# Optimization experiments

Measured on AMD Instinct MI355X. Metric: run time of the kernel, lower is better.

## Reference

```python
import jax, jax.numpy as jnp
import numpy as np

N = 100000
E = 1600000
D = 128  # out_dim == head_dim (num_heads = 1)


def setup_inputs() -> dict:
    key = jax.random.key(0)
    ks = jax.random.split(key, 16)
    s = 0.05
    inp = {
        "h": jax.random.normal(ks[0], (N, D), dtype=jnp.float32),
        "c": jax.random.normal(ks[1], (N, 3), dtype=jnp.float32),
        "src": jax.random.randint(ks[2], (E,), 0, N),
        "dst": jax.random.randint(ks[3], (E,), 0, N),
        # Q/K/V projections (use_bias=False)
        "Wq": jax.random.normal(ks[4], (D, D), dtype=jnp.float32) * s,
        "Wk": jax.random.normal(ks[5], (D, D), dtype=jnp.float32) * s,
        "Wv": jax.random.normal(ks[6], (D, D), dtype=jnp.float32) * s,
        # linear_p: Linear(3,3) -> ReLU -> Linear(3,D)
        "Wp1": jax.random.normal(ks[7], (3, 3), dtype=jnp.float32) * s,
        "bp1": jnp.zeros((3,), dtype=jnp.float32),
        "Wp2": jax.random.normal(ks[8], (3, D), dtype=jnp.float32) * s,
        "bp2": jnp.zeros((D,), dtype=jnp.float32),
        # edge MLP: Linear(D,D) -> ReLU -> Linear(D,1)
        "We1": jax.random.normal(ks[9], (D, D), dtype=jnp.float32) * s,
        "be1": jnp.zeros((D,), dtype=jnp.float32),
        "We2": jax.random.normal(ks[10], (D, 1), dtype=jnp.float32) * s,
        "be2": jnp.zeros((1,), dtype=jnp.float32),
        # output projection O (has bias)
        "Wo": jax.random.normal(ks[11], (D, D), dtype=jnp.float32) * s,
        "bo": jnp.zeros((D,), dtype=jnp.float32),
    }
    return inp


def reference(h, c, src, dst, Wq, Wk, Wv, Wp1, bp1, Wp2, bp2,
              We1, be1, We2, be2, Wo, bo):
    scale = np.sqrt(np.float32(D))  # sqrt(out_dim) used by scaled_exp
    n = h.shape[0]
    # node projections
    Q = h @ Wq                                   # [N, D]
    K = h @ Wk                                   # [N, D]
    V = h @ Wv                                   # [N, D]
    P = jax.nn.relu(c @ Wp1 + bp1) @ Wp2 + bp2   # [N, D] position encoding
    # per-edge point-transformer score: MLP(K[src] - Q[dst] + P[src])
    dif = K[src] - Q[dst] + P[src]               # [E, D]
    raw = jax.nn.relu(dif @ We1 + be1) @ We2 + be2  # [E, 1]
    score = jnp.exp(jnp.clip(raw / scale, -5.0, 5.0))  # [E, 1]
    # gather-multiply-scatter: weighted V+P sum and normalizer z per dst node
    msg = (V + P)[src] * score                   # [E, D]
    wV = jax.ops.segment_sum(msg, dst, num_segments=n)    # [N, D]
    z = jax.ops.segment_sum(score, dst, num_segments=n)   # [N, 1]
    head_out = wV / z                            # [N, D]
    return head_out @ Wo + bo                    # [N, D]
```

## Files before the change

### kernel.cpp

```cpp
#include <hip/hip_runtime.h>
#include <math.h>

#define DD 128
#define CAP 10240
#define KVS 272
typedef unsigned int u32;
typedef unsigned short u16;
typedef __attribute__((ext_vector_type(8))) short bf16x8;
typedef __attribute__((ext_vector_type(4))) float f32x4;
typedef __attribute__((ext_vector_type(2))) float f32x2;

__device__ __forceinline__ float4 f4zero() { return make_float4(0.f, 0.f, 0.f, 0.f); }
__device__ __forceinline__ u32 bf16rne(float f) {
    u32 u = __float_as_uint(f);
    u += 0x7FFFu + ((u >> 16) & 1u);
    return u >> 16;
}
__device__ __forceinline__ u32 pack2(float lo, float hi) {
    return bf16rne(lo) | (bf16rne(hi) << 16);
}
__device__ __forceinline__ float unlo(u32 u) { return __uint_as_float(u << 16); }
__device__ __forceinline__ float unhi(u32 u) { return __uint_as_float(u & 0xFFFF0000u); }
__device__ __forceinline__ float ub0(u32 v) { return (float)(v & 0xFFu); }
__device__ __forceinline__ float ub1(u32 v) { return (float)((v >> 8) & 0xFFu); }
__device__ __forceinline__ float ub2(u32 v) { return (float)((v >> 16) & 0xFFu); }
__device__ __forceinline__ float ub3(u32 v) { return (float)(v >> 24); }

__global__ __launch_bounds__(256) void fused_pre(
    const float* __restrict__ Wq, const float* __restrict__ Wk,
    const float* __restrict__ Wv, const float* __restrict__ We1,
    const float* __restrict__ be1, const float* __restrict__ Wp2,
    const float* __restrict__ bp2, const float* __restrict__ Wo,
    u32* __restrict__ BF,
    const int* __restrict__ src, const int* __restrict__ dst,
    int* __restrict__ gcount, u32* __restrict__ ebuf, int E) {
    const int t = threadIdx.x;
    if (blockIdx.x < 30) {
        const int bid = blockIdx.x * 4 + (t >> 6);
        const int l = t & 63;
        const int c = l & 15;
        const int kg = l >> 4;
        float val[8];

        const int ct = bid / 5, ks = bid - ct * 5;
        const int u = ct / 6, r = ct - u * 6;
        const int n = 32 * u + 16 * (r < 2 ? r : (r & 1)) + c;
#pragma unroll
        for (int j = 0; j < 8; ++j) {
            const int k = ks * 32 + kg * 8 + j;
            float v = 0.f;
            if (r < 2) {
                if (k < 128) {
                    float a = 0.f;
                    for (int q = 0; q < 128; ++q)
                        a = fmaf(Wq[k * 128 + q], We1[q * 128 + n], a);
                    v = a;
                }
            } else if (r < 4) {
                if (k < 128) {
                    float a = 0.f;
                    for (int q = 0; q < 128; ++q)
                        a = fmaf(Wk[k * 128 + q], We1[q * 128 + n], a);
                    v = a;
                } else if (k < 131) {
                    float a = 0.f;
                    for (int q = 0; q < 128; ++q)
                        a = fmaf(Wp2[(k - 128) * 128 + q], We1[q * 128 + n], a);
                    v = a;
                } else if (k == 131) {
                    float a = be1[n];
                    for (int q = 0; q < 128; ++q)
                        a = fmaf(bp2[q], We1[q * 128 + n], a);
                    v = a;
                }
            } else {
                if (k < 128) {
                    float a = 0.f;
                    for (int q = 0; q < 128; ++q)
                        a = fmaf(Wv[k * 128 + q], Wo[q * 128 + n], a);
                    v = a;
                } else if (k < 131) {
                    float a = 0.f;
                    for (int q = 0; q < 128; ++q)
                        a = fmaf(Wp2[(k - 128) * 128 + q], Wo[q * 128 + n], a);
                    v = a;
                } else if (k == 131) {
                    float a = 0.f;
                    for (int q = 0; q < 128; ++q)
                        a = fmaf(bp2[q], Wo[q * 128 + n], a);
                    v = a;
                }
            }
            val[j] = v;
        }
        u32* dp = &BF[((size_t)bid * 64 + l) * 4];
        dp[0] = pack2(val[0], val[1]);
        dp[1] = pack2(val[2], val[3]);
        dp[2] = pack2(val[4], val[5]);
        dp[3] = pack2(val[6], val[7]);
    } else {
        __shared__ int hist[256];
        __shared__ int base[256];
        hist[t] = 0;
        __syncthreads();
        const int chunk = (blockIdx.x - 30) * 4096;
        int bk[16], rk[16];
        u32 pv[16];
#pragma unroll
        for (int i = 0; i < 16; ++i) {
            int idx = chunk + i * 256 + t;
            bk[i] = -1;
            if (idx < E) {
                int dd = dst[idx];
                int ss = src[idx];
                bk[i] = dd >> 9;
                pv[i] = ((u32)ss << 9) | (u32)(dd & 511);
                rk[i] = atomicAdd(&hist[bk[i]], 1);
            }
        }
        __syncthreads();
        if (hist[t]) base[t] = t * CAP + atomicAdd(&gcount[t], hist[t]);
        __syncthreads();
#pragma unroll
        for (int i = 0; i < 16; ++i) {
            if (bk[i] >= 0) ebuf[base[bk[i]] + rk[i]] = pv[i];
        }
    }
}

__global__ __launch_bounds__(256) void scanB_we2r(
    const int* __restrict__ gcount, int* __restrict__ bucket_base,
    const float* __restrict__ We2, float* __restrict__ We2r) {
    __shared__ int s[256];
    int t = threadIdx.x;
    int orig = gcount[t];
    s[t] = orig;
    __syncthreads();
    for (int off = 1; off < 256; off <<= 1) {
        int x = (t >= off) ? s[t - off] : 0;
        __syncthreads();
        s[t] += x;
        __syncthreads();
    }
    bucket_base[t] = s[t] - orig;
    if (t < 128) {
        int col = 32 * (t >> 5) + 16 * (t & 1) + ((t & 31) >> 1);
        We2r[t] = We2[col];
    }
}

__global__ __launch_bounds__(256) void fused_mid(
    const float* __restrict__ h, const float* __restrict__ c,
    const float* __restrict__ Wp1, const float* __restrict__ bp1,
    const u32* __restrict__ BF,
    u32* __restrict__ QWb, unsigned char* __restrict__ KV, int N,
    const int* __restrict__ gcount, const int* __restrict__ bucket_base,
    const u32* __restrict__ ebuf, int* __restrict__ ssrc,
    int* __restrict__ offs, int E, int NR) {
    __shared__ u32 lds[64 * 96];
    const int t = threadIdx.x;

    if ((int)blockIdx.x < NR) {
        int* cnt = (int*)lds;
        int* cur = cnt + 512;
        int* ts = cur + 512;
        const int r = blockIdx.x;
        const int cnt_r = gcount[r];
        const int base_r = bucket_base[r];
        cnt[t] = 0;
        cnt[t + 256] = 0;
        __syncthreads();
        const u32* eb = &ebuf[(size_t)r * CAP];
        for (int i = t; i < cnt_r; i += 256) atomicAdd(&cnt[eb[i] & 511], 1);
        __syncthreads();
        int v0 = cnt[2 * t], v1 = cnt[2 * t + 1];
        int pair = v0 + v1;
        ts[t] = pair;
        __syncthreads();
        for (int off = 1; off < 256; off <<= 1) {
            int x = (t >= off) ? ts[t - off] : 0;
            __syncthreads();
            ts[t] += x;
            __syncthreads();
        }
        int ex = ts[t] - pair;
        cur[2 * t] = ex;
        cur[2 * t + 1] = ex + v0;
        offs[r * 512 + 2 * t] = base_r + ex;
        offs[r * 512 + 2 * t + 1] = base_r + ex + v0;
        if (r == NR - 1 && t == 255) offs[NR * 512] = E;
        __syncthreads();
        for (int i = t; i < cnt_r; i += 256) {
            u32 e = eb[i];
            int p = atomicAdd(&cur[e & 511], 1);
            ssrc[base_r + p] = (int)(e >> 9);
        }
    } else {
        u32* hs = lds;
        const int row0 = ((int)blockIdx.x - NR) * 64;

#pragma unroll
        for (int i = 0; i < 8; ++i) {
            int f = t + i * 256;
            int row = f >> 5;
            int cq = f & 31;
            float4 v = f4zero();
            if (row0 + row < N) v = *(const float4*)&h[(size_t)(row0 + row) * DD + cq * 4];
            int idx = row * 96 + ((cq * 2) ^ ((row & 7) << 2));
            uint2 p;
            p.x = pack2(v.x, v.y);
            p.y = pack2(v.z, v.w);
            *(uint2*)&hs[idx] = p;
        }
        if (t < 64) {
            int row = t;
            float u0 = 0.f, u1 = 0.f, u2 = 0.f;
            if (row0 + row < N) {
                const float* cr = &c[(size_t)(row0 + row) * 3];
                float c0 = cr[0], c1 = cr[1], c2 = cr[2];
                u0 = fmaxf(bp1[0] + c0 * Wp1[0] + c1 * Wp1[3] + c2 * Wp1[6], 0.f);
                u1 = fmaxf(bp1[1] + c0 * Wp1[1] + c1 * Wp1[4] + c2 * Wp1[7], 0.f);
                u2 = fmaxf(bp1[2] + c0 * Wp1[2] + c1 * Wp1[5] + c2 * Wp1[8], 0.f);
            }
            int swz = (row & 7) << 2;
            uint4 z0 = make_uint4(pack2(u0, u1), pack2(u2, 1.0f), 0u, 0u);
            uint4 zz = make_uint4(0u, 0u, 0u, 0u);
#pragma unroll
            for (int q = 0; q < 4; ++q) {
                int idx = row * 96 + 64 + ((q * 4) ^ swz);
                *(uint4*)&hs[idx] = (q == 0) ? z0 : zz;
            }
        }
        __syncthreads();

        const int w = t >> 6, l = t & 63;
        const int cc = l & 15, kg = l >> 4;

        f32x4 acc[4][6];
#pragma unroll
        for (int rt = 0; rt < 4; ++rt)
#pragma unroll
            for (int r = 0; r < 6; ++r) acc[rt][r] = (f32x4){0.f, 0.f, 0.f, 0.f};

#pragma unroll
        for (int ks = 0; ks < 5; ++ks) {
            bf16x8 a[4];
#pragma unroll
            for (int rt = 0; rt < 4; ++rt) {
                int row = rt * 16 + cc;
                int idx = row * 96 + ((ks * 16 + kg * 4) ^ ((row & 7) << 2));
                a[rt] = *(const bf16x8*)&hs[idx];
            }
#pragma unroll
            for (int r = 0; r < 6; ++r) {
                const bf16x8 b = *(const bf16x8*)&BF[(((size_t)(w * 6 + r) * 5 + ks) * 64 + l) * 4];
#pragma unroll
                for (int rt = 0; rt < 4; ++rt)
                    acc[rt][r] = __builtin_amdgcn_mfma_f32_16x16x32_bf16(a[rt], b, acc[rt][r], 0, 0, 0);
            }
        }

        __syncthreads();
        if (t < 64) hs[t] = 0u;
        __syncthreads();
#pragma unroll
        for (int rt = 0; rt < 4; ++rt) {
#pragma unroll
            for (int j = 0; j < 4; ++j) {
                int rl = rt * 16 + kg * 4 + j;
                float m = fmaxf(fabsf(acc[rt][4][j]), fabsf(acc[rt][5][j]));
                atomicMax((int*)&hs[rl], __float_as_int(m));
            }
        }
        __syncthreads();

#pragma unroll
        for (int rt = 0; rt < 4; ++rt) {
#pragma unroll
            for (int j = 0; j < 4; ++j) {
                int rl = rt * 16 + kg * 4 + j;
                int row = row0 + rl;
                if (row >= N) continue;
                float smax = __int_as_float((int)hs[rl]);
                float scale = (smax > 0.f) ? smax * (1.0f / 127.0f) : 1.0f;
                float rsc = 1.0f / scale;
                QWb[(size_t)row * 64 + w * 16 + cc] = pack2(acc[rt][0][j], acc[rt][1][j]);
                unsigned char* kvrow = &KV[(size_t)row * KVS];
                u32 kp = __builtin_amdgcn_cvt_pk_fp8_f32(acc[rt][2][j], acc[rt][3][j], 0u, false);
                *(u16*)&kvrow[w * 32 + cc * 2] = (u16)kp;
                int q0 = (int)rintf(acc[rt][4][j] * rsc) + 128;
                int q1 = (int)rintf(acc[rt][5][j] * rsc) + 128;
                *(u16*)&kvrow[128 + 2 * (w * 16 + cc)] = (u16)((q0 & 0xFF) | ((q1 & 0xFF) << 8));
                if (w == 0 && cc == 0) *(float*)&kvrow[256] = scale;
            }
        }
    }
}

__global__ __launch_bounds__(256) void aggregate(
    const int* __restrict__ offs, const int* __restrict__ ssrc,
    const unsigned char* __restrict__ KV, const u32* __restrict__ QWb,
    const float* __restrict__ We2r, const float* __restrict__ be2,
    const float* __restrict__ bo, float* __restrict__ out, int N) {
    const int node = (blockIdx.x * 256 + threadIdx.x) >> 6;
    const int lane = threadIdx.x & 63;
    if (node >= N) return;
    const int g = lane >> 4, i = lane & 15;

    const float SC = 0.08838834764831845f * 1.4426950408889634f;
    const float CL = 5.0f * 1.4426950408889634f;

    uint4 Qu = *(const uint4*)&QWb[(size_t)node * 64 + 4 * i];
    f32x2 q01 = {unlo(Qu.x), unhi(Qu.x)};
    f32x2 q23 = {unlo(Qu.y), unhi(Qu.y)};
    f32x2 q45 = {unlo(Qu.z), unhi(Qu.z)};
    f32x2 q67 = {unlo(Qu.w), unhi(Qu.w)};
    f32x2 w01 = *(const f32x2*)&We2r[8 * i];
    f32x2 w23 = *(const f32x2*)&We2r[8 * i + 2];
    f32x2 w45 = *(const f32x2*)&We2r[8 * i + 4];
    f32x2 w67 = *(const f32x2*)&We2r[8 * i + 6];
    const float B2SC = be2[0] * SC;
    const f32x2 zero2 = {0.f, 0.f};

    const int beg = offs[node], end = offs[node + 1];
    float a0 = 0.f, a1 = 0.f, a2 = 0.f, a3 = 0.f;
    float a4 = 0.f, a5 = 0.f, a6 = 0.f, a7 = 0.f;
    float zacc = 0.f, zs = 0.f;

    int e = beg + g;
    int s = (e < end) ? ssrc[e] : 0;
    for (int e0 = beg; e0 < end; e0 += 4) {
        const bool act = (e0 + g) < end;
        const unsigned char* row = &KV[(size_t)s * KVS];
        uint2 kk = *(const uint2*)&row[8 * i];
        uint2 vv = *(const uint2*)&row[128 + 8 * i];
        float scl = *(const float*)&row[256];
        int en = e0 + 4 + g;
        s = (en < end) ? ssrc[en] : 0;

        f32x2 d, p2;
        d = __builtin_amdgcn_cvt_pk_f32_fp8(kk.x, false) - q01;
        d = __builtin_elementwise_max(d, zero2);
        p2 = d * w01;
        d = __builtin_amdgcn_cvt_pk_f32_fp8(kk.x, true) - q23;
        d = __builtin_elementwise_max(d, zero2);
        p2 += d * w23;
        d = __builtin_amdgcn_cvt_pk_f32_fp8(kk.y, false) - q45;
        d = __builtin_elementwise_max(d, zero2);
        p2 += d * w45;
        d = __builtin_amdgcn_cvt_pk_f32_fp8(kk.y, true) - q67;
        d = __builtin_elementwise_max(d, zero2);
        p2 += d * w67;
        float p = p2[0] + p2[1];
#pragma unroll
        for (int off = 1; off <= 8; off <<= 1) p += __shfl_xor(p, off);

        float targ = fmaf(p, SC, B2SC);
        targ = fminf(fmaxf(targ, -CL), CL);
        float sc = act ? exp2f(targ) : 0.f;
        float scsc = sc * scl;
        zacc += sc;
        zs += scsc;

        a0 = fmaf(ub0(vv.x), scsc, a0);
        a1 = fmaf(ub1(vv.x), scsc, a1);
        a2 = fmaf(ub2(vv.x), scsc, a2);
        a3 = fmaf(ub3(vv.x), scsc, a3);
        a4 = fmaf(ub0(vv.y), scsc, a4);
        a5 = fmaf(ub1(vv.y), scsc, a5);
        a6 = fmaf(ub2(vv.y), scsc, a6);
        a7 = fmaf(ub3(vv.y), scsc, a7);
    }

    a0 += __shfl_xor(a0, 16); a0 += __shfl_xor(a0, 32);
    a1 += __shfl_xor(a1, 16); a1 += __shfl_xor(a1, 32);
    a2 += __shfl_xor(a2, 16); a2 += __shfl_xor(a2, 32);
    a3 += __shfl_xor(a3, 16); a3 += __shfl_xor(a3, 32);
    a4 += __shfl_xor(a4, 16); a4 += __shfl_xor(a4, 32);
    a5 += __shfl_xor(a5, 16); a5 += __shfl_xor(a5, 32);
    a6 += __shfl_xor(a6, 16); a6 += __shfl_xor(a6, 32);
    a7 += __shfl_xor(a7, 16); a7 += __shfl_xor(a7, 32);
    zacc += __shfl_xor(zacc, 16); zacc += __shfl_xor(zacc, 32);
    zs += __shfl_xor(zs, 16); zs += __shfl_xor(zs, 32);

    if (g == 0) {
        float corr = 128.0f * zs;
        float rz = 1.0f / zacc;
        const int base = 32 * (i >> 2) + 4 * (i & 3);
        float4 bA = *(const float4*)&bo[base];
        float4 bB = *(const float4*)&bo[base + 16];
        float4 oA = make_float4(fmaf(a0 - corr, rz, bA.x), fmaf(a2 - corr, rz, bA.y),
                                fmaf(a4 - corr, rz, bA.z), fmaf(a6 - corr, rz, bA.w));
        float4 oB = make_float4(fmaf(a1 - corr, rz, bB.x), fmaf(a3 - corr, rz, bB.y),
                                fmaf(a5 - corr, rz, bB.z), fmaf(a7 - corr, rz, bB.w));
        float* orow = &out[(size_t)node * DD];
        *(float4*)&orow[base] = oA;
        *(float4*)&orow[base + 16] = oB;
    }
}

extern "C" void kernel_launch(void* const* d_in, const int* in_sizes, int n_in,
                              void* d_out, int out_size, void* d_ws, size_t ws_size,
                              hipStream_t stream) {
    const float* h   = (const float*)d_in[0];
    const float* c   = (const float*)d_in[1];
    const int*   src = (const int*)d_in[2];
    const int*   dst = (const int*)d_in[3];
    const float* Wq  = (const float*)d_in[4];
    const float* Wk  = (const float*)d_in[5];
    const float* Wv  = (const float*)d_in[6];
    const float* Wp1 = (const float*)d_in[7];
    const float* bp1 = (const float*)d_in[8];
    const float* Wp2 = (const float*)d_in[9];
    const float* bp2 = (const float*)d_in[10];
    const float* We1 = (const float*)d_in[11];
    const float* be1 = (const float*)d_in[12];
    const float* We2 = (const float*)d_in[13];
    const float* be2 = (const float*)d_in[14];
    const float* Wo  = (const float*)d_in[15];
    const float* bo  = (const float*)d_in[16];

    const int N = in_sizes[0] / DD;
    const int E = in_sizes[2];
    const int NR = (N + 511) >> 9;
    const int NB1 = (E + 4095) / 4096;
    const int NG = (N + 63) / 64;

    u32* BF    = (u32*)d_ws;
    u32* QWb   = BF + 120 * 256;
    unsigned char* KV = (unsigned char*)(QWb + (size_t)N * 64);
    int* offs  = (int*)(KV + (size_t)N * KVS);
    int* gcount = offs + ((size_t)NR * 512 + 1);
    int* bbase  = gcount + 256;
    float* We2r = (float*)(bbase + 256);
    int* ssrc   = (int*)(We2r + 128);
    u32* ebuf   = (u32*)(ssrc + E);

    hipMemsetAsync(gcount, 0, 256 * sizeof(int), stream);

    fused_pre<<<30 + NB1, 256, 0, stream>>>(Wq, Wk, Wv, We1, be1, Wp2, bp2, Wo,
                                            BF, src, dst, gcount, ebuf, E);

    scanB_we2r<<<1, 256, 0, stream>>>(gcount, bbase, We2, We2r);

    fused_mid<<<NR + NG, 256, 0, stream>>>(
        h, c, Wp1, bp1, BF, QWb, KV, N,
        gcount, bbase, ebuf, ssrc, offs, E, NR);

    aggregate<<<(N * 64 + 255) / 256, 256, 0, stream>>>(
        offs, ssrc, KV, QWb, We2r, be2, bo, (float*)d_out, N);
}
```

Before: 203.4 us.

## Use per-8-column int8 V scales in a separate buffer and shrink KV rows

The V int8 quantization scale changes from one per row to one per group of 8 columns. Each group's max is reduced with lane shuffles instead of LDS atomics and two block barriers. The scales move to a separate Sb buffer of 16 floats per node, so the KV row shrinks from 272 to 256 bytes and aligns better for the random gathers in aggregate. The trade-off is a second gather per edge from the scale buffer, and the finer-grained scales also change quantization accuracy.

```diff
diff --git a/kernel.cpp b/kernel.cpp
--- a/kernel.cpp
+++ b/kernel.cpp
@@ -3,7 +3,7 @@
 
 #define DD 128
 #define CAP 10240
-#define KVS 272
+#define KVS 256
 typedef unsigned int u32;
 typedef unsigned short u16;
 typedef __attribute__((ext_vector_type(8))) short bf16x8;
@@ -153,7 +153,8 @@
     const float* __restrict__ h, const float* __restrict__ c,
     const float* __restrict__ Wp1, const float* __restrict__ bp1,
     const u32* __restrict__ BF,
-    u32* __restrict__ QWb, unsigned char* __restrict__ KV, int N,
+    u32* __restrict__ QWb, unsigned char* __restrict__ KV,
+    float* __restrict__ Sb, int N,
     const int* __restrict__ gcount, const int* __restrict__ bucket_base,
     const u32* __restrict__ ebuf, int* __restrict__ ssrc,
     int* __restrict__ offs, int E, int NR) {
@@ -260,29 +261,16 @@
             }
         }
 
-        __syncthreads();
-        if (t < 64) hs[t] = 0u;
-        __syncthreads();
 #pragma unroll
         for (int rt = 0; rt < 4; ++rt) {
 #pragma unroll
             for (int j = 0; j < 4; ++j) {
-                int rl = rt * 16 + kg * 4 + j;
+                int row = row0 + rt * 16 + kg * 4 + j;
                 float m = fmaxf(fabsf(acc[rt][4][j]), fabsf(acc[rt][5][j]));
-                atomicMax((int*)&hs[rl], __float_as_int(m));
-            }
-        }
-        __syncthreads();
-
-#pragma unroll
-        for (int rt = 0; rt < 4; ++rt) {
-#pragma unroll
-            for (int j = 0; j < 4; ++j) {
-                int rl = rt * 16 + kg * 4 + j;
-                int row = row0 + rl;
+                m = fmaxf(m, __shfl_xor(m, 1));
+                m = fmaxf(m, __shfl_xor(m, 2));
                 if (row >= N) continue;
-                float smax = __int_as_float((int)hs[rl]);
-                float scale = (smax > 0.f) ? smax * (1.0f / 127.0f) : 1.0f;
+                float scale = (m > 0.f) ? m * (1.0f / 127.0f) : 1.0f;
                 float rsc = 1.0f / scale;
                 QWb[(size_t)row * 64 + w * 16 + cc] = pack2(acc[rt][0][j], acc[rt][1][j]);
                 unsigned char* kvrow = &KV[(size_t)row * KVS];
@@ -291,7 +279,8 @@
                 int q0 = (int)rintf(acc[rt][4][j] * rsc) + 128;
                 int q1 = (int)rintf(acc[rt][5][j] * rsc) + 128;
                 *(u16*)&kvrow[128 + 2 * (w * 16 + cc)] = (u16)((q0 & 0xFF) | ((q1 & 0xFF) << 8));
-                if (w == 0 && cc == 0) *(float*)&kvrow[256] = scale;
+                if ((cc & 3) == 0)
+                    Sb[(size_t)row * 16 + 4 * w + (cc >> 2)] = scale;
             }
         }
     }
@@ -299,9 +288,10 @@
 
 __global__ __launch_bounds__(256) void aggregate(
     const int* __restrict__ offs, const int* __restrict__ ssrc,
-    const unsigned char* __restrict__ KV, const u32* __restrict__ QWb,
-    const float* __restrict__ We2r, const float* __restrict__ be2,
-    const float* __restrict__ bo, float* __restrict__ out, int N) {
+    const unsigned char* __restrict__ KV, const float* __restrict__ Sb,
+    const u32* __restrict__ QWb, const float* __restrict__ We2r,
+    const float* __restrict__ be2, const float* __restrict__ bo,
+    float* __restrict__ out, int N) {
     const int node = (blockIdx.x * 256 + threadIdx.x) >> 6;
     const int lane = threadIdx.x & 63;
     if (node >= N) return;
@@ -334,7 +324,7 @@
         const unsigned char* row = &KV[(size_t)s * KVS];
         uint2 kk = *(const uint2*)&row[8 * i];
         uint2 vv = *(const uint2*)&row[128 + 8 * i];
-        float scl = *(const float*)&row[256];
+        float scl = Sb[(size_t)s * 16 + i];
         int en = e0 + 4 + g;
         s = (en < end) ? ssrc[en] : 0;
 
@@ -429,7 +419,8 @@
     u32* BF    = (u32*)d_ws;
     u32* QWb   = BF + 120 * 256;
     unsigned char* KV = (unsigned char*)(QWb + (size_t)N * 64);
-    int* offs  = (int*)(KV + (size_t)N * KVS);
+    float* Sb  = (float*)(KV + (size_t)N * KVS);
+    int* offs  = (int*)(Sb + (size_t)N * 16);
     int* gcount = offs + ((size_t)NR * 512 + 1);
     int* bbase  = gcount + 256;
     float* We2r = (float*)(bbase + 256);
@@ -444,9 +435,9 @@
     scanB_we2r<<<1, 256, 0, stream>>>(gcount, bbase, We2, We2r);
 
     fused_mid<<<NR + NG, 256, 0, stream>>>(
-        h, c, Wp1, bp1, BF, QWb, KV, N,
+        h, c, Wp1, bp1, BF, QWb, KV, Sb, N,
         gcount, bbase, ebuf, ssrc, offs, E, NR);
 
     aggregate<<<(N * 64 + 255) / 256, 256, 0, stream>>>(
-        offs, ssrc, KV, QWb, We2r, be2, bo, (float*)d_out, N);
-}
+        offs, ssrc, KV, Sb, QWb, We2r, be2, bo, (float*)d_out, N);
+}
```

Measured after the change: 199.2 us. 2.1% less time.
